# Kernel tuning notes

Measured on AMD Instinct MI355X. Metric: run time of the kernel, lower is better.

Reference implementation:

```python
import jax, jax.numpy as jnp
import numpy as np

B, S, D = 4, 4096, 256

def setup_inputs() -> dict:
    key = jax.random.key(0)
    k1, k2, k3, k4 = jax.random.split(key, 4)
    inputs = jax.random.normal(k1, (B, S, D), dtype=jnp.float32)
    Wq = jax.random.normal(k2, (D, D), dtype=jnp.float32) * 0.05
    Wk = jax.random.normal(k3, (D, D), dtype=jnp.float32) * 0.05
    Wv = jax.random.normal(k4, (D, D), dtype=jnp.float32) * 0.05
    return {"inputs": inputs, "Wq": Wq, "Wk": Wk, "Wv": Wv}

def reference(inputs, Wq, Wk, Wv):
    # single-head self-attention: softmax(QK^T / sqrt(d)) V
    d = inputs.shape[-1]
    Q = jnp.einsum('bsd,de->bse', inputs, Wq)
    K = jnp.einsum('bsd,de->bse', inputs, Wk)
    V = jnp.einsum('bsd,de->bse', inputs, Wv)
    scale = 1.0 / jnp.sqrt(jnp.asarray(d, dtype=inputs.dtype))
    scores = jnp.einsum('bqe,bke->bqk', Q, K) * scale  # [B,S,S]
    attn = jax.nn.softmax(scores, axis=-1)
    return jnp.einsum('bqk,bke->bqe', attn, V)
```

## Files before the change

kernel.cpp:

```cpp
#include <hip/hip_runtime.h>
#include <hip/hip_bf16.h>

typedef __attribute__((ext_vector_type(8))) short bfrag_t;
typedef __attribute__((ext_vector_type(4))) short s4_t;
typedef __attribute__((ext_vector_type(4))) float facc_t;
typedef __attribute__((ext_vector_type(16))) float f16acc_t;
typedef __attribute__((ext_vector_type(4))) int i4_t;

#define B_ 4
#define S_ 4096
#define D_ 256

using gas_v = const __attribute__((address_space(1))) void;
using las_v = __attribute__((address_space(3))) void;

__device__ __forceinline__ short f2bf(float f) {
  union { float fv; unsigned u; } x; x.fv = f;
  unsigned r = x.u + 0x7FFFu + ((x.u >> 16) & 1u);
  return (short)(r >> 16);
}

__device__ __forceinline__ int cvtpk(float lo, float hi) {
  int r;
  asm("v_cvt_pk_bf16_f32 %0, %1, %2" : "=v"(r) : "v"(lo), "v"(hi));
  return r;
}

__device__ __forceinline__ facc_t mfma16(bfrag_t a, bfrag_t b, facc_t c) {
  return __builtin_amdgcn_mfma_f32_16x16x32_bf16(a, b, c, 0, 0, 0);
}
__device__ __forceinline__ f16acc_t mfma32(bfrag_t a, bfrag_t b, f16acc_t c) {
  return __builtin_amdgcn_mfma_f32_32x32x16_bf16(a, b, c, 0, 0, 0);
}

__global__ void wt_kernel(const float* __restrict__ Wq, const float* __restrict__ Wk,
                          const float* __restrict__ Wv, short* __restrict__ WT) {
  const int p = blockIdx.x >> 4;
  const float* W = (p == 0) ? Wq : ((p == 1) ? Wk : Wv);
  short* o = WT + p * (D_ * D_);
  const int e = (blockIdx.x & 15) * 16 + (threadIdx.x >> 4);
  const int td = threadIdx.x & 15;
  #pragma unroll
  for (int dd = 0; dd < 16; ++dd) {
    int d = td * 16 + dd;
    o[e * D_ + d] = f2bf(W[d * D_ + e]);
  }
}

__global__ __launch_bounds__(256) void proj_kernel(
    const float* __restrict__ X, const short* __restrict__ WT,
    short* __restrict__ Qb, short* __restrict__ Kb, short* __restrict__ VT) {
  __shared__ __align__(16) short Stg[256 * 72];
  const int tid  = threadIdx.x;
  const int wave = tid >> 6, lane = tid & 63;
  const int lrow = lane & 15, kch = lane >> 4;
  const int rb = blockIdx.x;
  const int row0 = rb * 64 + wave * 16;
  const int arow = row0 + lrow;
  const int bblk = rb >> 6;

  bfrag_t af[8];
  #pragma unroll
  for (int kt = 0; kt < 8; ++kt) {
    const float* src = X + (size_t)arow * D_ + kt * 32 + kch * 8;
    float4 a = *reinterpret_cast<const float4*>(src);
    float4 b = *reinterpret_cast<const float4*>(src + 4);
    bfrag_t f;
    f[0] = f2bf(a.x); f[1] = f2bf(a.y); f[2] = f2bf(a.z); f[3] = f2bf(a.w);
    f[4] = f2bf(b.x); f[5] = f2bf(b.y); f[6] = f2bf(b.z); f[7] = f2bf(b.w);
    af[kt] = f;
  }

  #pragma unroll 1
  for (int p = 0; p < 3; ++p) {
    const short* Wp = WT + p * (D_ * D_);
    facc_t acc[16];
    #pragma unroll
    for (int nt = 0; nt < 16; ++nt) acc[nt] = (facc_t)0.0f;
    #pragma unroll
    for (int kt = 0; kt < 8; ++kt) {
      #pragma unroll
      for (int nt = 0; nt < 16; ++nt) {
        bfrag_t bf = *reinterpret_cast<const bfrag_t*>(
            Wp + (nt * 16 + lrow) * D_ + kt * 32 + kch * 8);
        acc[nt] = mfma16(af[kt], bf, acc[nt]);
      }
    }
    __syncthreads();
    if (p < 2) {
      const float sc = (p == 0) ? 0.0625f : 1.0f;
      #pragma unroll
      for (int nt = 0; nt < 16; ++nt)
        #pragma unroll
        for (int r = 0; r < 4; ++r)
          Stg[(wave * 16 + kch * 4 + r) * 264 + nt * 16 + lrow] =
              f2bf(acc[nt][r] * sc);
      __syncthreads();
      short* dstbase = ((p == 0) ? Qb : Kb) + (size_t)rb * 64 * D_;
      #pragma unroll
      for (int k = 0; k < 8; ++k) {
        int c = k * 256 + tid;
        int row = c >> 5, col = c & 31;
        *reinterpret_cast<bfrag_t*>(dstbase + row * D_ + col * 8) =
            *reinterpret_cast<const bfrag_t*>(&Stg[row * 264 + col * 8]);
      }
    } else {
      #pragma unroll
      for (int nt = 0; nt < 16; ++nt) {
        s4_t v;
        #pragma unroll
        for (int r = 0; r < 4; ++r) v[r] = f2bf(acc[nt][r]);
        *reinterpret_cast<s4_t*>(
            &Stg[(nt * 16 + lrow) * 72 + (wave >> 1) * 32 + (wave & 1) * 16 +
                 (kch & 1) * 8 + (kch >> 1) * 4]) = v;
      }
      __syncthreads();
      const int d = tid;
      const int s0 = (rb & 63) * 64;
      short* dst = VT + ((size_t)(bblk * D_ + d)) * S_ + s0;
      #pragma unroll
      for (int j = 0; j < 8; ++j)
        *reinterpret_cast<bfrag_t*>(dst + j * 8) =
            *reinterpret_cast<const bfrag_t*>(&Stg[d * 72 + j * 8]);
    }
  }
}

template<int SPLIT>
__global__ __launch_bounds__(512, 2) void attn32(
    const short* __restrict__ Qb, const short* __restrict__ Kb,
    const short* __restrict__ VT, float* __restrict__ P0,
    float* __restrict__ PX, float2* __restrict__ ML) {
  __shared__ __align__(16) short Kl[3][32 * 256];
  __shared__ __align__(16) short Vl[3][256 * 32];
  const int tid  = threadIdx.x;
  const int wave = tid >> 6, lane = tid & 63;
  const int l31 = lane & 31, hi = lane >> 5;
  const int ksw = (lane & 7) << 4;
  const int vsw = ((l31 >> 1) & 3) << 4;
  const int hw = blockIdx.x;
  const int xcd = hw & 7, i = hw >> 3;
  int b, part, qblk;
  if constexpr (SPLIT == 4) {
    int combo = (i & 1) * 8 + xcd;
    b = combo >> 2; part = combo & 3; qblk = i >> 1;
  } else if constexpr (SPLIT == 2) {
    b = xcd >> 1; part = xcd & 1; qblk = i;
  } else {
    b = hw >> 4; part = 0; qblk = hw & 15;
  }
  const int q0 = qblk * 256 + wave * 32;
  const int kvbase = part * (S_ / SPLIT);
  constexpr int STEPS = (S_ / SPLIT) / 32;

  const short* Kbp = Kb + (size_t)b * S_ * D_ + (size_t)kvbase * D_;
  const short* Vbp = VT + (size_t)b * D_ * S_ + kvbase;

  bfrag_t qf[16];
  const short* Qp = Qb + ((size_t)b * S_ + q0 + l31) * D_;
  #pragma unroll
  for (int kt = 0; kt < 16; ++kt)
    qf[kt] = *reinterpret_cast<const bfrag_t*>(Qp + kt * 16 + hi * 8);

  auto stage = [&](int bf, int kv0) {
    #pragma unroll
    for (int j = 0; j < 2; ++j) {
      int L = j * 8192 + tid * 16;
      int row = L >> 9;
      int cs = (L & 511) ^ ((row & 7) << 4);
      const short* src = Kbp + (size_t)(kv0 + row) * D_ + (cs >> 1);
      short* dst = &Kl[bf][(j * 8192 + wave * 1024) >> 1];
      __builtin_amdgcn_global_load_lds((gas_v*)src, (las_v*)dst, 16, 0, 0);
    }
    #pragma unroll
    for (int j = 0; j < 2; ++j) {
      int L = j * 8192 + tid * 16;
      int d = L >> 6;
      int cs = (L & 63) ^ (((d >> 1) & 3) << 4);
      const short* src = Vbp + (size_t)d * S_ + kv0 + (cs >> 1);
      short* dst = &Vl[bf][(j * 8192 + wave * 1024) >> 1];
      __builtin_amdgcn_global_load_lds((gas_v*)src, (las_v*)dst, 16, 0, 0);
    }
  };

  f16acc_t o32[8];
  #pragma unroll
  for (int nt = 0; nt < 8; ++nt) o32[nt] = (f16acc_t)0.0f;
  float mrow = -3.0e38f, lsum = 0.0f;

  stage(0, 0);
  stage(1, 32);

  #pragma unroll 1
  for (int t = 0; t < STEPS; ++t) {
    const int buf = t % 3;
    if (t < STEPS - 1) {
      asm volatile("s_waitcnt vmcnt(4)" ::: "memory");
    } else {
      asm volatile("s_waitcnt vmcnt(0)" ::: "memory");
    }
    __builtin_amdgcn_sched_barrier(0);
    __builtin_amdgcn_s_barrier();
    __builtin_amdgcn_sched_barrier(0);
    if (t + 2 < STEPS) stage((t + 2) % 3, (t + 2) * 32);
    f16acc_t s16 = (f16acc_t)0.0f;
    const char* Kbase = (const char*)&Kl[buf][0];
    __builtin_amdgcn_s_setprio(1);
    #pragma unroll
    for (int kt = 0; kt < 16; ++kt) {
      bfrag_t kf = *reinterpret_cast<const bfrag_t*>(
          Kbase + l31 * 512 + ((kt * 32 + hi * 16) ^ ksw));
      s16 = mfma32(kf, qf[kt], s16);
    }
    __builtin_amdgcn_s_setprio(0);
    float mx = s16[0];
    #pragma unroll
    for (int i2 = 1; i2 < 16; ++i2) mx = fmaxf(mx, s16[i2]);
    mx = fmaxf(mx, __shfl_xor(mx, 32));
    if (mx > mrow + 8.0f) {
      float sf = __expf(mrow - mx);
      mrow = mx;
      lsum *= sf;
      #pragma unroll
      for (int nt = 0; nt < 8; ++nt) o32[nt] *= sf;
    }
    float ls = 0.0f;
    #pragma unroll
    for (int i2 = 0; i2 < 16; ++i2) {
      float e = __expf(s16[i2] - mrow);
      s16[i2] = e;
      ls += e;
    }
    lsum += ls;
    i4_t w0, w1;
    w0.x = cvtpk(s16[0], s16[1]);   w0.y = cvtpk(s16[2], s16[3]);
    w0.z = cvtpk(s16[4], s16[5]);   w0.w = cvtpk(s16[6], s16[7]);
    w1.x = cvtpk(s16[8], s16[9]);   w1.y = cvtpk(s16[10], s16[11]);
    w1.z = cvtpk(s16[12], s16[13]); w1.w = cvtpk(s16[14], s16[15]);
    bfrag_t pb0 = __builtin_bit_cast(bfrag_t, w0);
    bfrag_t pb1 = __builtin_bit_cast(bfrag_t, w1);
    const char* Vbase = (const char*)&Vl[buf][0];
    __builtin_amdgcn_s_setprio(1);
    #pragma unroll
    for (int nt = 0; nt < 8; ++nt) {
      const char* vb = Vbase + (nt * 32 + l31) * 64;
      bfrag_t v0 = *reinterpret_cast<const bfrag_t*>(vb + ((hi * 16) ^ vsw));
      o32[nt] = mfma32(v0, pb0, o32[nt]);
      bfrag_t v1 = *reinterpret_cast<const bfrag_t*>(vb + ((32 + hi * 16) ^ vsw));
      o32[nt] = mfma32(v1, pb1, o32[nt]);
    }
    __builtin_amdgcn_s_setprio(0);
  }

  lsum += __shfl_xor(lsum, 32);
  float* Pd = (SPLIT == 1 || part == 0)
                  ? P0 : PX + (size_t)(part - 1) * ((size_t)B_ * S_ * D_);
  float* Og = Pd + ((size_t)b * S_ + q0 + l31) * D_;
  if constexpr (SPLIT == 1) {
    float inv = 1.0f / lsum;
    #pragma unroll
    for (int nt = 0; nt < 8; ++nt)
      #pragma unroll
      for (int gg = 0; gg < 4; ++gg) {
        float4 o;
        o.x = o32[nt][gg * 4 + 0] * inv; o.y = o32[nt][gg * 4 + 1] * inv;
        o.z = o32[nt][gg * 4 + 2] * inv; o.w = o32[nt][gg * 4 + 3] * inv;
        *reinterpret_cast<float4*>(Og + nt * 32 + hi * 4 + gg * 8) = o;
      }
  } else {
    #pragma unroll
    for (int nt = 0; nt < 8; ++nt)
      #pragma unroll
      for (int gg = 0; gg < 4; ++gg) {
        float4 o;
        o.x = o32[nt][gg * 4 + 0]; o.y = o32[nt][gg * 4 + 1];
        o.z = o32[nt][gg * 4 + 2]; o.w = o32[nt][gg * 4 + 3];
        *reinterpret_cast<float4*>(Og + nt * 32 + hi * 4 + gg * 8) = o;
      }
    if (lane < 32) {
      float2 ml; ml.x = mrow; ml.y = lsum;
      ML[part * (B_ * S_) + b * S_ + q0 + l31] = ml;
    }
  }
}

template<int SPLIT>
__global__ __launch_bounds__(256) void combineN(
    const float* __restrict__ PX, const float2* __restrict__ ML,
    float* __restrict__ Out) {
  const int r = blockIdx.x * 4 + (threadIdx.x >> 6);
  const int d4 = (threadIdx.x & 63) * 4;
  float2 ml[SPLIT];
  #pragma unroll
  for (int p = 0; p < SPLIT; ++p) ml[p] = ML[p * (B_ * S_) + r];
  float m = ml[0].x;
  #pragma unroll
  for (int p = 1; p < SPLIT; ++p) m = fmaxf(m, ml[p].x);
  float w[SPLIT];
  float denom = 0.0f;
  #pragma unroll
  for (int p = 0; p < SPLIT; ++p) {
    w[p] = __expf(ml[p].x - m);
    denom += ml[p].y * w[p];
  }
  float inv = 1.0f / denom;
  size_t idx = (size_t)r * D_ + d4;
  float4 x = *reinterpret_cast<float4*>(Out + idx);
  float4 acc;
  acc.x = x.x * w[0]; acc.y = x.y * w[0]; acc.z = x.z * w[0]; acc.w = x.w * w[0];
  #pragma unroll
  for (int p = 1; p < SPLIT; ++p) {
    float4 y = *reinterpret_cast<const float4*>(
        PX + (size_t)(p - 1) * ((size_t)B_ * S_ * D_) + idx);
    acc.x += y.x * w[p]; acc.y += y.y * w[p];
    acc.z += y.z * w[p]; acc.w += y.w * w[p];
  }
  acc.x *= inv; acc.y *= inv; acc.z *= inv; acc.w *= inv;
  *reinterpret_cast<float4*>(Out + idx) = acc;
}

extern "C" void kernel_launch(void* const* d_in, const int* in_sizes, int n_in,
                              void* d_out, int out_size, void* d_ws, size_t ws_size,
                              hipStream_t stream) {
  const float* X  = (const float*)d_in[0];
  const float* Wq = (const float*)d_in[1];
  const float* Wk = (const float*)d_in[2];
  const float* Wv = (const float*)d_in[3];
  float* out = (float*)d_out;

  char* ws = (char*)d_ws;
  short* Qb = (short*)(ws);
  short* Kb = (short*)(ws + 8388608);
  short* VT = (short*)(ws + 16777216);
  short* WT = (short*)(ws + 25165824);
  float2* ML = (float2*)(ws + 25690112);
  float* PX  = (float*)(ws + 26214400);
  const size_t NP = (size_t)B_ * S_ * D_ * 4;
  const size_t need4 = 26214400 + 3 * NP;
  const size_t need2 = 26214400 + 1 * NP;

  wt_kernel<<<48, 256, 0, stream>>>(Wq, Wk, Wv, WT);
  proj_kernel<<<256, 256, 0, stream>>>(X, WT, Qb, Kb, VT);
  if (ws_size >= need4) {
    attn32<4><<<256, 512, 0, stream>>>(Qb, Kb, VT, out, PX, ML);
    combineN<4><<<(B_ * S_) / 4, 256, 0, stream>>>(PX, ML, out);
  } else if (ws_size >= need2) {
    attn32<2><<<128, 512, 0, stream>>>(Qb, Kb, VT, out, PX, ML);
    combineN<2><<<(B_ * S_) / 4, 256, 0, stream>>>(PX, ML, out);
  } else {
    attn32<1><<<64, 512, 0, stream>>>(Qb, Kb, VT, out, PX, (float2*)out);
  }
}
```

Before: 157.0 us.

## Process two query tiles per wave in attention and split projection across blocks

The attention kernel now runs 4 waves of 256 threads, with each wave handling 64 query rows as two 32-row tiles. Each K/V fragment read from LDS is reused for two MFMAs, halving LDS traffic per unit of compute, and the staging loops and waitcnt are adjusted for the smaller block. The projection kernel launches three times as many blocks, one per Q/K/V projection, to raise parallelism at the cost of re-reading and re-converting X for each. Register pressure roughly doubles for accumulators and Q fragments, and the setprio hints are removed, which may hurt occupancy or scheduling.

```diff
diff --git a/kernel.cpp b/kernel.cpp
--- a/kernel.cpp
+++ b/kernel.cpp
@@ -54,7 +54,8 @@
   const int tid  = threadIdx.x;
   const int wave = tid >> 6, lane = tid & 63;
   const int lrow = lane & 15, kch = lane >> 4;
-  const int rb = blockIdx.x;
+  const int p  = blockIdx.x >> 8;
+  const int rb = blockIdx.x & 255;
   const int row0 = rb * 64 + wave * 16;
   const int arow = row0 + lrow;
   const int bblk = rb >> 6;
@@ -71,63 +72,59 @@
     af[kt] = f;
   }
 
-  #pragma unroll 1
-  for (int p = 0; p < 3; ++p) {
-    const short* Wp = WT + p * (D_ * D_);
-    facc_t acc[16];
-    #pragma unroll
-    for (int nt = 0; nt < 16; ++nt) acc[nt] = (facc_t)0.0f;
-    #pragma unroll
-    for (int kt = 0; kt < 8; ++kt) {
-      #pragma unroll
-      for (int nt = 0; nt < 16; ++nt) {
-        bfrag_t bf = *reinterpret_cast<const bfrag_t*>(
-            Wp + (nt * 16 + lrow) * D_ + kt * 32 + kch * 8);
-        acc[nt] = mfma16(af[kt], bf, acc[nt]);
-      }
-    }
+  const short* Wp = WT + p * (D_ * D_);
+  facc_t acc[16];
+  #pragma unroll
+  for (int nt = 0; nt < 16; ++nt) acc[nt] = (facc_t)0.0f;
+  #pragma unroll
+  for (int kt = 0; kt < 8; ++kt) {
+    #pragma unroll
+    for (int nt = 0; nt < 16; ++nt) {
+      bfrag_t bf = *reinterpret_cast<const bfrag_t*>(
+          Wp + (nt * 16 + lrow) * D_ + kt * 32 + kch * 8);
+      acc[nt] = mfma16(af[kt], bf, acc[nt]);
+    }
+  }
+  if (p < 2) {
+    const float sc = (p == 0) ? 0.0625f : 1.0f;
+    #pragma unroll
+    for (int nt = 0; nt < 16; ++nt)
+      #pragma unroll
+      for (int r = 0; r < 4; ++r)
+        Stg[(wave * 16 + kch * 4 + r) * 264 + nt * 16 + lrow] =
+            f2bf(acc[nt][r] * sc);
     __syncthreads();
-    if (p < 2) {
-      const float sc = (p == 0) ? 0.0625f : 1.0f;
-      #pragma unroll
-      for (int nt = 0; nt < 16; ++nt)
-        #pragma unroll
-        for (int r = 0; r < 4; ++r)
-          Stg[(wave * 16 + kch * 4 + r) * 264 + nt * 16 + lrow] =
-              f2bf(acc[nt][r] * sc);
-      __syncthreads();
-      short* dstbase = ((p == 0) ? Qb : Kb) + (size_t)rb * 64 * D_;
-      #pragma unroll
-      for (int k = 0; k < 8; ++k) {
-        int c = k * 256 + tid;
-        int row = c >> 5, col = c & 31;
-        *reinterpret_cast<bfrag_t*>(dstbase + row * D_ + col * 8) =
-            *reinterpret_cast<const bfrag_t*>(&Stg[row * 264 + col * 8]);
-      }
-    } else {
-      #pragma unroll
-      for (int nt = 0; nt < 16; ++nt) {
-        s4_t v;
-        #pragma unroll
-        for (int r = 0; r < 4; ++r) v[r] = f2bf(acc[nt][r]);
-        *reinterpret_cast<s4_t*>(
-            &Stg[(nt * 16 + lrow) * 72 + (wave >> 1) * 32 + (wave & 1) * 16 +
-                 (kch & 1) * 8 + (kch >> 1) * 4]) = v;
-      }
-      __syncthreads();
-      const int d = tid;
-      const int s0 = (rb & 63) * 64;
-      short* dst = VT + ((size_t)(bblk * D_ + d)) * S_ + s0;
-      #pragma unroll
-      for (int j = 0; j < 8; ++j)
-        *reinterpret_cast<bfrag_t*>(dst + j * 8) =
-            *reinterpret_cast<const bfrag_t*>(&Stg[d * 72 + j * 8]);
-    }
+    short* dstbase = ((p == 0) ? Qb : Kb) + (size_t)rb * 64 * D_;
+    #pragma unroll
+    for (int k = 0; k < 8; ++k) {
+      int c = k * 256 + tid;
+      int row = c >> 5, col = c & 31;
+      *reinterpret_cast<bfrag_t*>(dstbase + row * D_ + col * 8) =
+          *reinterpret_cast<const bfrag_t*>(&Stg[row * 264 + col * 8]);
+    }
+  } else {
+    #pragma unroll
+    for (int nt = 0; nt < 16; ++nt) {
+      s4_t v;
+      #pragma unroll
+      for (int r = 0; r < 4; ++r) v[r] = f2bf(acc[nt][r]);
+      *reinterpret_cast<s4_t*>(
+          &Stg[(nt * 16 + lrow) * 72 + (wave >> 1) * 32 + (wave & 1) * 16 +
+               (kch & 1) * 8 + (kch >> 1) * 4]) = v;
+    }
+    __syncthreads();
+    const int d = tid;
+    const int s0 = (rb & 63) * 64;
+    short* dst = VT + ((size_t)(bblk * D_ + d)) * S_ + s0;
+    #pragma unroll
+    for (int j = 0; j < 8; ++j)
+      *reinterpret_cast<bfrag_t*>(dst + j * 8) =
+          *reinterpret_cast<const bfrag_t*>(&Stg[d * 72 + j * 8]);
   }
 }
 
 template<int SPLIT>
-__global__ __launch_bounds__(512, 2) void attn32(
+__global__ __launch_bounds__(256, 1) void attn32(
     const short* __restrict__ Qb, const short* __restrict__ Kb,
     const short* __restrict__ VT, float* __restrict__ P0,
     float* __restrict__ PX, float2* __restrict__ ML) {
@@ -149,44 +146,48 @@
   } else {
     b = hw >> 4; part = 0; qblk = hw & 15;
   }
-  const int q0 = qblk * 256 + wave * 32;
+  const int q0 = qblk * 256 + wave * 64;
   const int kvbase = part * (S_ / SPLIT);
   constexpr int STEPS = (S_ / SPLIT) / 32;
 
   const short* Kbp = Kb + (size_t)b * S_ * D_ + (size_t)kvbase * D_;
   const short* Vbp = VT + (size_t)b * D_ * S_ + kvbase;
 
-  bfrag_t qf[16];
-  const short* Qp = Qb + ((size_t)b * S_ + q0 + l31) * D_;
-  #pragma unroll
-  for (int kt = 0; kt < 16; ++kt)
-    qf[kt] = *reinterpret_cast<const bfrag_t*>(Qp + kt * 16 + hi * 8);
+  bfrag_t qf[16], qg[16];
+  const short* Qp0 = Qb + ((size_t)b * S_ + q0 + l31) * D_;
+  const short* Qp1 = Qp0 + 32 * D_;
+  #pragma unroll
+  for (int kt = 0; kt < 16; ++kt) {
+    qf[kt] = *reinterpret_cast<const bfrag_t*>(Qp0 + kt * 16 + hi * 8);
+    qg[kt] = *reinterpret_cast<const bfrag_t*>(Qp1 + kt * 16 + hi * 8);
+  }
 
   auto stage = [&](int bf, int kv0) {
     #pragma unroll
-    for (int j = 0; j < 2; ++j) {
-      int L = j * 8192 + tid * 16;
+    for (int j = 0; j < 4; ++j) {
+      int L = j * 4096 + tid * 16;
       int row = L >> 9;
       int cs = (L & 511) ^ ((row & 7) << 4);
       const short* src = Kbp + (size_t)(kv0 + row) * D_ + (cs >> 1);
-      short* dst = &Kl[bf][(j * 8192 + wave * 1024) >> 1];
+      short* dst = &Kl[bf][(j * 4096 + wave * 1024) >> 1];
       __builtin_amdgcn_global_load_lds((gas_v*)src, (las_v*)dst, 16, 0, 0);
     }
     #pragma unroll
-    for (int j = 0; j < 2; ++j) {
-      int L = j * 8192 + tid * 16;
+    for (int j = 0; j < 4; ++j) {
+      int L = j * 4096 + tid * 16;
       int d = L >> 6;
       int cs = (L & 63) ^ (((d >> 1) & 3) << 4);
       const short* src = Vbp + (size_t)d * S_ + kv0 + (cs >> 1);
-      short* dst = &Vl[bf][(j * 8192 + wave * 1024) >> 1];
+      short* dst = &Vl[bf][(j * 4096 + wave * 1024) >> 1];
       __builtin_amdgcn_global_load_lds((gas_v*)src, (las_v*)dst, 16, 0, 0);
     }
   };
 
-  f16acc_t o32[8];
-  #pragma unroll
-  for (int nt = 0; nt < 8; ++nt) o32[nt] = (f16acc_t)0.0f;
-  float mrow = -3.0e38f, lsum = 0.0f;
+  f16acc_t oA[8], oB[8];
+  #pragma unroll
+  for (int nt = 0; nt < 8; ++nt) { oA[nt] = (f16acc_t)0.0f; oB[nt] = (f16acc_t)0.0f; }
+  float mA = -3.0e38f, lA = 0.0f;
+  float mB = -3.0e38f, lB = 0.0f;
 
   stage(0, 0);
   stage(1, 32);
@@ -195,7 +196,7 @@
   for (int t = 0; t < STEPS; ++t) {
     const int buf = t % 3;
     if (t < STEPS - 1) {
-      asm volatile("s_waitcnt vmcnt(4)" ::: "memory");
+      asm volatile("s_waitcnt vmcnt(8)" ::: "memory");
     } else {
       asm volatile("s_waitcnt vmcnt(0)" ::: "memory");
     }
@@ -203,69 +204,100 @@
     __builtin_amdgcn_s_barrier();
     __builtin_amdgcn_sched_barrier(0);
     if (t + 2 < STEPS) stage((t + 2) % 3, (t + 2) * 32);
-    f16acc_t s16 = (f16acc_t)0.0f;
+    f16acc_t sA = (f16acc_t)0.0f, sB = (f16acc_t)0.0f;
     const char* Kbase = (const char*)&Kl[buf][0];
-    __builtin_amdgcn_s_setprio(1);
     #pragma unroll
     for (int kt = 0; kt < 16; ++kt) {
       bfrag_t kf = *reinterpret_cast<const bfrag_t*>(
           Kbase + l31 * 512 + ((kt * 32 + hi * 16) ^ ksw));
-      s16 = mfma32(kf, qf[kt], s16);
-    }
-    __builtin_amdgcn_s_setprio(0);
-    float mx = s16[0];
-    #pragma unroll
-    for (int i2 = 1; i2 < 16; ++i2) mx = fmaxf(mx, s16[i2]);
-    mx = fmaxf(mx, __shfl_xor(mx, 32));
-    if (mx > mrow + 8.0f) {
-      float sf = __expf(mrow - mx);
-      mrow = mx;
-      lsum *= sf;
-      #pragma unroll
-      for (int nt = 0; nt < 8; ++nt) o32[nt] *= sf;
-    }
-    float ls = 0.0f;
-    #pragma unroll
-    for (int i2 = 0; i2 < 16; ++i2) {
-      float e = __expf(s16[i2] - mrow);
-      s16[i2] = e;
-      ls += e;
-    }
-    lsum += ls;
-    i4_t w0, w1;
-    w0.x = cvtpk(s16[0], s16[1]);   w0.y = cvtpk(s16[2], s16[3]);
-    w0.z = cvtpk(s16[4], s16[5]);   w0.w = cvtpk(s16[6], s16[7]);
-    w1.x = cvtpk(s16[8], s16[9]);   w1.y = cvtpk(s16[10], s16[11]);
-    w1.z = cvtpk(s16[12], s16[13]); w1.w = cvtpk(s16[14], s16[15]);
-    bfrag_t pb0 = __builtin_bit_cast(bfrag_t, w0);
-    bfrag_t pb1 = __builtin_bit_cast(bfrag_t, w1);
+      sA = mfma32(kf, qf[kt], sA);
+      sB = mfma32(kf, qg[kt], sB);
+    }
+    bfrag_t pb0, pb1, pb2, pb3;
+    {
+      float mx = sA[0];
+      #pragma unroll
+      for (int i2 = 1; i2 < 16; ++i2) mx = fmaxf(mx, sA[i2]);
+      mx = fmaxf(mx, __shfl_xor(mx, 32));
+      if (mx > mA + 8.0f) {
+        float sf = __expf(mA - mx);
+        mA = mx; lA *= sf;
+        #pragma unroll
+        for (int nt = 0; nt < 8; ++nt) oA[nt] *= sf;
+      }
+      float ls = 0.0f;
+      #pragma unroll
+      for (int i2 = 0; i2 < 16; ++i2) {
+        float e = __expf(sA[i2] - mA);
+        sA[i2] = e; ls += e;
+      }
+      lA += ls;
+      i4_t w0, w1;
+      w0.x = cvtpk(sA[0], sA[1]);   w0.y = cvtpk(sA[2], sA[3]);
+      w0.z = cvtpk(sA[4], sA[5]);   w0.w = cvtpk(sA[6], sA[7]);
+      w1.x = cvtpk(sA[8], sA[9]);   w1.y = cvtpk(sA[10], sA[11]);
+      w1.z = cvtpk(sA[12], sA[13]); w1.w = cvtpk(sA[14], sA[15]);
+      pb0 = __builtin_bit_cast(bfrag_t, w0);
+      pb1 = __builtin_bit_cast(bfrag_t, w1);
+    }
+    {
+      float mx = sB[0];
+      #pragma unroll
+      for (int i2 = 1; i2 < 16; ++i2) mx = fmaxf(mx, sB[i2]);
+      mx = fmaxf(mx, __shfl_xor(mx, 32));
+      if (mx > mB + 8.0f) {
+        float sf = __expf(mB - mx);
+        mB = mx; lB *= sf;
+        #pragma unroll
+        for (int nt = 0; nt < 8; ++nt) oB[nt] *= sf;
+      }
+      float ls = 0.0f;
+      #pragma unroll
+      for (int i2 = 0; i2 < 16; ++i2) {
+        float e = __expf(sB[i2] - mB);
+        sB[i2] = e; ls += e;
+      }
+      lB += ls;
+      i4_t w0, w1;
+      w0.x = cvtpk(sB[0], sB[1]);   w0.y = cvtpk(sB[2], sB[3]);
+      w0.z = cvtpk(sB[4], sB[5]);   w0.w = cvtpk(sB[6], sB[7]);
+      w1.x = cvtpk(sB[8], sB[9]);   w1.y = cvtpk(sB[10], sB[11]);
+      w1.z = cvtpk(sB[12], sB[13]); w1.w = cvtpk(sB[14], sB[15]);
+      pb2 = __builtin_bit_cast(bfrag_t, w0);
+      pb3 = __builtin_bit_cast(bfrag_t, w1);
+    }
     const char* Vbase = (const char*)&Vl[buf][0];
-    __builtin_amdgcn_s_setprio(1);
     #pragma unroll
     for (int nt = 0; nt < 8; ++nt) {
       const char* vb = Vbase + (nt * 32 + l31) * 64;
       bfrag_t v0 = *reinterpret_cast<const bfrag_t*>(vb + ((hi * 16) ^ vsw));
-      o32[nt] = mfma32(v0, pb0, o32[nt]);
       bfrag_t v1 = *reinterpret_cast<const bfrag_t*>(vb + ((32 + hi * 16) ^ vsw));
-      o32[nt] = mfma32(v1, pb1, o32[nt]);
-    }
-    __builtin_amdgcn_s_setprio(0);
-  }
-
-  lsum += __shfl_xor(lsum, 32);
+      oA[nt] = mfma32(v0, pb0, oA[nt]);
+      oA[nt] = mfma32(v1, pb1, oA[nt]);
+      oB[nt] = mfma32(v0, pb2, oB[nt]);
+      oB[nt] = mfma32(v1, pb3, oB[nt]);
+    }
+  }
+
+  lA += __shfl_xor(lA, 32);
+  lB += __shfl_xor(lB, 32);
   float* Pd = (SPLIT == 1 || part == 0)
                   ? P0 : PX + (size_t)(part - 1) * ((size_t)B_ * S_ * D_);
-  float* Og = Pd + ((size_t)b * S_ + q0 + l31) * D_;
+  float* Og0 = Pd + ((size_t)b * S_ + q0 + l31) * D_;
+  float* Og1 = Og0 + 32 * D_;
   if constexpr (SPLIT == 1) {
-    float inv = 1.0f / lsum;
+    float ivA = 1.0f / lA, ivB = 1.0f / lB;
     #pragma unroll
     for (int nt = 0; nt < 8; ++nt)
       #pragma unroll
       for (int gg = 0; gg < 4; ++gg) {
         float4 o;
-        o.x = o32[nt][gg * 4 + 0] * inv; o.y = o32[nt][gg * 4 + 1] * inv;
-        o.z = o32[nt][gg * 4 + 2] * inv; o.w = o32[nt][gg * 4 + 3] * inv;
-        *reinterpret_cast<float4*>(Og + nt * 32 + hi * 4 + gg * 8) = o;
+        o.x = oA[nt][gg * 4 + 0] * ivA; o.y = oA[nt][gg * 4 + 1] * ivA;
+        o.z = oA[nt][gg * 4 + 2] * ivA; o.w = oA[nt][gg * 4 + 3] * ivA;
+        *reinterpret_cast<float4*>(Og0 + nt * 32 + hi * 4 + gg * 8) = o;
+        o.x = oB[nt][gg * 4 + 0] * ivB; o.y = oB[nt][gg * 4 + 1] * ivB;
+        o.z = oB[nt][gg * 4 + 2] * ivB; o.w = oB[nt][gg * 4 + 3] * ivB;
+        *reinterpret_cast<float4*>(Og1 + nt * 32 + hi * 4 + gg * 8) = o;
       }
   } else {
     #pragma unroll
@@ -273,13 +305,18 @@
       #pragma unroll
       for (int gg = 0; gg < 4; ++gg) {
         float4 o;
-        o.x = o32[nt][gg * 4 + 0]; o.y = o32[nt][gg * 4 + 1];
-        o.z = o32[nt][gg * 4 + 2]; o.w = o32[nt][gg * 4 + 3];
-        *reinterpret_cast<float4*>(Og + nt * 32 + hi * 4 + gg * 8) = o;
+        o.x = oA[nt][gg * 4 + 0]; o.y = oA[nt][gg * 4 + 1];
+        o.z = oA[nt][gg * 4 + 2]; o.w = oA[nt][gg * 4 + 3];
+        *reinterpret_cast<float4*>(Og0 + nt * 32 + hi * 4 + gg * 8) = o;
+        o.x = oB[nt][gg * 4 + 0]; o.y = oB[nt][gg * 4 + 1];
+        o.z = oB[nt][gg * 4 + 2]; o.w = oB[nt][gg * 4 + 3];
+        *reinterpret_cast<float4*>(Og1 + nt * 32 + hi * 4 + gg * 8) = o;
       }
     if (lane < 32) {
-      float2 ml; ml.x = mrow; ml.y = lsum;
-      ML[part * (B_ * S_) + b * S_ + q0 + l31] = ml;
+      float2 ml0; ml0.x = mA; ml0.y = lA;
+      ML[part * (B_ * S_) + b * S_ + q0 + l31] = ml0;
+      float2 ml1; ml1.x = mB; ml1.y = lB;
+      ML[part * (B_ * S_) + b * S_ + q0 + 32 + l31] = ml1;
     }
   }
 }
@@ -340,14 +377,14 @@
   const size_t need2 = 26214400 + 1 * NP;
 
   wt_kernel<<<48, 256, 0, stream>>>(Wq, Wk, Wv, WT);
-  proj_kernel<<<256, 256, 0, stream>>>(X, WT, Qb, Kb, VT);
+  proj_kernel<<<768, 256, 0, stream>>>(X, WT, Qb, Kb, VT);
   if (ws_size >= need4) {
-    attn32<4><<<256, 512, 0, stream>>>(Qb, Kb, VT, out, PX, ML);
+    attn32<4><<<256, 256, 0, stream>>>(Qb, Kb, VT, out, PX, ML);
     combineN<4><<<(B_ * S_) / 4, 256, 0, stream>>>(PX, ML, out);
   } else if (ws_size >= need2) {
-    attn32<2><<<128, 512, 0, stream>>>(Qb, Kb, VT, out, PX, ML);
+    attn32<2><<<128, 256, 0, stream>>>(Qb, Kb, VT, out, PX, ML);
     combineN<2><<<(B_ * S_) / 4, 256, 0, stream>>>(PX, ML, out);
   } else {
-    attn32<1><<<64, 512, 0, stream>>>(Qb, Kb, VT, out, PX, (float2*)out);
-  }
-}
+    attn32<1><<<64, 256, 0, stream>>>(Qb, Kb, VT, out, PX, (float2*)out);
+  }
+}
```

Result: slower. 578.7 us (+268.7%).
